# Performance work log

Hardware: AMD Instinct MI355X
Metric: run time of the kernel (lower is better)

Reference implementation:

```python
import jax, jax.numpy as jnp
import numpy as np

N, E, HD, ED = 8000, 40000, 64, 16


def setup_inputs() -> dict:
    key = jax.random.key(0)
    ks = jax.random.split(key, 10)
    def nrm(k, shp, s):
        return jax.random.normal(k, shp, dtype=jnp.float32) * s
    return {
        "x": jax.random.normal(ks[0], (N, HD), dtype=jnp.float32),
        "edge_attr": jax.random.uniform(ks[1], (E, ED), dtype=jnp.float32),
        "W1": nrm(ks[2], (ED, HD), 0.2),
        "b1": jnp.zeros((HD,), jnp.float32),
        "W2": nrm(ks[3], (HD, HD * HD), 0.05),
        "b2": jnp.zeros((HD * HD,), jnp.float32),
        "W_root": nrm(ks[4], (HD, HD), 0.1),
        "b_conv": jnp.zeros((HD,), jnp.float32),
        "w_ih": nrm(ks[5], (3 * HD, HD), 0.1),
        "w_hh": nrm(ks[6], (3 * HD, HD), 0.1),
        "b_ih": jnp.zeros((3 * HD,), jnp.float32),
        "b_hh": jnp.zeros((3 * HD,), jnp.float32),
        "edge_index": jax.random.randint(ks[7], (2, E), 0, N),
    }


def reference(x, edge_attr, W1, b1, W2, b2, W_root, b_conv, w_ih, w_hh, b_ih, b_hh, edge_index):
    src, dst = edge_index[0], edge_index[1]
    n_nodes, hd = x.shape
    n_edges = edge_attr.shape[0]
    # in-degree counts for scatter-mean (guard against isolated nodes)
    counts = jnp.maximum(
        jax.ops.segment_sum(jnp.ones((n_edges,), x.dtype), dst, num_segments=n_nodes), 1.0
    )
    # edge MLP -> per-edge [hd, hd] weight; edge_attr is loop-invariant so compute once
    Wedge = (jax.nn.relu(edge_attr @ W1 + b1) @ W2 + b2).reshape(n_edges, hd, hd)

    def gru_cell(m, h):
        gi = m @ w_ih.T + b_ih  # [N, 3h], gate order r,z,n (torch layout)
        gh = h @ w_hh.T + b_hh
        i_r, i_z, i_n = jnp.split(gi, 3, axis=-1)
        h_r, h_z, h_n = jnp.split(gh, 3, axis=-1)
        r = jax.nn.sigmoid(i_r + h_r)
        z = jax.nn.sigmoid(i_z + h_z)
        n = jnp.tanh(i_n + r * h_n)
        return (1.0 - z) * n + z * h

    out = x
    hidden = x  # h = out.unsqueeze(0)
    for _ in range(3):
        # NNConv: gather source feats, per-edge matmul, scatter-mean to target
        msg = jnp.einsum('ei,eio->eo', out[src], Wedge)  # [E, hd]
        agg = jax.ops.segment_sum(msg, dst, num_segments=n_nodes) / counts[:, None]
        m = jax.nn.relu(agg + out @ W_root.T + b_conv)
        hidden = gru_cell(m, hidden)
        out = hidden  # GRU output == new hidden for seq_len 1
    return out
```

## Files before the change

### kernel.cpp

```cpp
#include <hip/hip_runtime.h>

#define HD 64
#define ED 16

typedef __bf16 bf16x8 __attribute__((ext_vector_type(8)));
typedef float  f32x4  __attribute__((ext_vector_type(4)));
typedef unsigned int u32;
typedef unsigned long long u64;
typedef unsigned short u16;

static inline __device__ float bf2f(u16 u){
    union { u32 i; float f; } v; v.i = ((u32)u) << 16; return v.f;
}
static inline __device__ u16 f2bf(float f){
    union { u32 i; float f; } v; v.f = f;
    u32 r = v.i + 0x7FFF + ((v.i >> 16) & 1);
    return (u16)(r >> 16);
}
static inline __device__ u32 pk2(float a, float b){
    return (u32)f2bf(a) | ((u32)f2bf(b) << 16);
}

__global__ void k_zero2(int* a, int* b, int n){
    int i = blockIdx.x*blockDim.x + threadIdx.x;
    if(i < n){ a[i] = 0; b[i] = 0; }
}
__global__ void k_deg(const int* __restrict__ src, const int* __restrict__ dst, int E,
                      int* __restrict__ degs, int* __restrict__ degd){
    int e = blockIdx.x*blockDim.x + threadIdx.x;
    if(e < E){ atomicAdd(&degs[src[e]], 1); atomicAdd(&degd[dst[e]], 1); }
}

__global__ void k_scan(const int* __restrict__ degs, const int* __restrict__ degd, int N,
                       int* __restrict__ rowptr, int* __restrict__ cursor, float* __restrict__ countsf){
    __shared__ int part[1024];
    int tid = threadIdx.x;
    int PER = (N + 1023) >> 10;
    int base = tid * PER;
    int local[16];
    int s = 0;
    for(int j = 0; j < PER; j++){
        int idx = base + j;
        int v = (idx < N) ? degs[idx] : 0;
        local[j] = s; s += v;
    }
    part[tid] = s;
    __syncthreads();
    for(int off = 1; off < 1024; off <<= 1){
        int v = (tid >= off) ? part[tid - off] : 0;
        __syncthreads();
        part[tid] += v;
        __syncthreads();
    }
    int prev = (tid == 0) ? 0 : part[tid - 1];
    for(int j = 0; j < PER; j++){
        int idx = base + j;
        if(idx < N){
            int r = prev + local[j];
            rowptr[idx] = r; cursor[idx] = r;
            int dd = degd[idx];
            countsf[idx] = (dd > 0) ? (float)dd : 1.0f;
        }
    }
    if(tid == 1023) rowptr[N] = prev + s;
}

__global__ void k_fill(const int* __restrict__ src, int E, int* __restrict__ cursor, int* __restrict__ elist){
    int e = blockIdx.x*blockDim.x + threadIdx.x;
    if(e < E){ int p = atomicAdd(&cursor[src[e]], 1); elist[p] = e; }
}

__global__ void k_h1E(const float* __restrict__ ea, const float* __restrict__ W1,
                      const float* __restrict__ b1, const int* __restrict__ elist,
                      const int* __restrict__ dstarr, int E,
                      u16* __restrict__ h1E, int* __restrict__ dstE){
    __shared__ float s_ea[4][ED];
    __shared__ int s_e[4];
    int t = threadIdx.x;
    int o = t & 63, el = t >> 6;
    int p = blockIdx.x*4 + el;
    if(t < 4){
        int pp = blockIdx.x*4 + t;
        s_e[t] = (pp < E) ? elist[pp] : 0;
    }
    __syncthreads();
    if(t < 4*ED){
        int pe = t/ED;
        s_ea[pe][t%ED] = ea[(size_t)s_e[pe]*ED + t%ED];
    }
    __syncthreads();
    if(p < E){
        float acc = b1[o];
        #pragma unroll
        for(int k = 0; k < ED; k++) acc += s_ea[el][k] * W1[k*HD + o];
        h1E[(size_t)p*HD + o] = f2bf(acc > 0.f ? acc : 0.f);
        if(o == 0) dstE[p] = dstarr[s_e[el]];
    }
}

#define SEG_PT   (65*HD*HD)
#define SEG_WIH  (3*HD*HD)
#define SEG_WHH  (3*HD*HD)
#define SEG_WR   (HD*HD)
__global__ void k_prep(const float* __restrict__ W2, const float* __restrict__ b2,
                       const float* __restrict__ w_ih, const float* __restrict__ w_hh,
                       const float* __restrict__ Wroot, const float* __restrict__ x,
                       u16* __restrict__ PT, u16* __restrict__ WihB, u16* __restrict__ WhhB,
                       u16* __restrict__ WrB, u16* __restrict__ Abf, int nx){
    int idx = blockIdx.x*blockDim.x + threadIdx.x;
    if(idx < SEG_PT){
        int c = idx / HD, i = idx % HD;
        int kc = c >> 6, o = c & 63;
        float v = (kc < HD) ? W2[(size_t)kc*(HD*HD) + i*HD + o] : b2[i*HD + o];
        PT[idx] = f2bf(v);
        return;
    }
    idx -= SEG_PT;
    if(idx < SEG_WIH){ WihB[idx] = f2bf(w_ih[idx]); return; }
    idx -= SEG_WIH;
    if(idx < SEG_WHH){ WhhB[idx] = f2bf(w_hh[idx]); return; }
    idx -= SEG_WHH;
    if(idx < SEG_WR){ WrB[idx] = f2bf(Wroot[idx]); return; }
    idx -= SEG_WR;
    if(idx < nx) Abf[idx] = f2bf(x[idx]);
}

static __device__ __forceinline__ void mfma_row(const u16* __restrict__ Pb,
        int r, int g, bf16x8 a0, bf16x8 a1, f32x4* acc){
    #pragma unroll
    for(int cb = 0; cb < 4; cb++){
        bf16x8 b0 = *(const bf16x8*)&Pb[(cb*16 + r)*HD + g*8];
        bf16x8 b1 = *(const bf16x8*)&Pb[(cb*16 + r)*HD + 32 + g*8];
        acc[cb] = __builtin_amdgcn_mfma_f32_16x16x32_bf16(a0, b0, acc[cb], 0,0,0);
        acc[cb] = __builtin_amdgcn_mfma_f32_16x16x32_bf16(a1, b1, acc[cb], 0,0,0);
    }
}

__global__ __launch_bounds__(256) void k_gemmA4(
        const u16* __restrict__ Abf, const u16* __restrict__ PT,
        u16* __restrict__ Mt, float* __restrict__ Mb, float* __restrict__ agg, int N){
    __shared__ u16 sP[4*HD*HD];
    int t = threadIdx.x;
    int Q = blockIdx.x;
    if(Q == 16){
        int stride = gridDim.y * 256;
        f32x4 z = (f32x4){0.f,0.f,0.f,0.f};
        for(int i = blockIdx.y*256 + t; i < N*HD/4; i += stride)
            *(f32x4*)&agg[i*4] = z;
        return;
    }
    int w = t >> 6, lane = t & 63;
    int r = lane & 15, g = lane >> 4;
    int n0 = (blockIdx.y * 4 + w) * 16;
    size_t NQ = (size_t)N * 256;

    bf16x8 a0 = *(const bf16x8*)&Abf[(size_t)(n0 + r)*HD + g*8];
    bf16x8 a1 = *(const bf16x8*)&Abf[(size_t)(n0 + r)*HD + 32 + g*8];

    {
        const uint4* src = (const uint4*)(PT + (size_t)(Q*4)*HD*HD);
        uint4 tmp0 = src[0*256 + t], tmp1 = src[1*256 + t],
              tmp2 = src[2*256 + t], tmp3 = src[3*256 + t],
              tmp4 = src[4*256 + t], tmp5 = src[5*256 + t],
              tmp6 = src[6*256 + t], tmp7 = src[7*256 + t];
        #define STG(rd, val) { int idx = (rd)*256 + t; int row = idx >> 3, sl = idx & 7; \
            *(uint4*)((char*)sP + row*128 + ((sl ^ (row&7))<<4)) = (val); }
        STG(0, tmp0) STG(1, tmp1) STG(2, tmp2) STG(3, tmp3)
        STG(4, tmp4) STG(5, tmp5) STG(6, tmp6) STG(7, tmp7)
        #undef STG
    }
    __syncthreads();

    f32x4 acc0[4], acc1[4], acc2[4], acc3[4];
    #pragma unroll
    for(int cb = 0; cb < 4; cb++){
        acc0[cb] = (f32x4){0.f,0.f,0.f,0.f};
        acc1[cb] = (f32x4){0.f,0.f,0.f,0.f};
        acc2[cb] = (f32x4){0.f,0.f,0.f,0.f};
        acc3[cb] = (f32x4){0.f,0.f,0.f,0.f};
    }
    #define LDB(j, cb, ks) (*(const bf16x8*)((const char*)sP + \
        ((j)*64 + (cb)*16 + r)*128 + ((((ks)*4 + g) ^ (((cb)*16 + r)&7))<<4)))
    #pragma unroll
    for(int cb = 0; cb < 4; cb++){
        acc0[cb] = __builtin_amdgcn_mfma_f32_16x16x32_bf16(a0, LDB(0,cb,0), acc0[cb], 0,0,0);
        acc0[cb] = __builtin_amdgcn_mfma_f32_16x16x32_bf16(a1, LDB(0,cb,1), acc0[cb], 0,0,0);
        acc1[cb] = __builtin_amdgcn_mfma_f32_16x16x32_bf16(a0, LDB(1,cb,0), acc1[cb], 0,0,0);
        acc1[cb] = __builtin_amdgcn_mfma_f32_16x16x32_bf16(a1, LDB(1,cb,1), acc1[cb], 0,0,0);
        acc2[cb] = __builtin_amdgcn_mfma_f32_16x16x32_bf16(a0, LDB(2,cb,0), acc2[cb], 0,0,0);
        acc2[cb] = __builtin_amdgcn_mfma_f32_16x16x32_bf16(a1, LDB(2,cb,1), acc2[cb], 0,0,0);
        acc3[cb] = __builtin_amdgcn_mfma_f32_16x16x32_bf16(a0, LDB(3,cb,0), acc3[cb], 0,0,0);
        acc3[cb] = __builtin_amdgcn_mfma_f32_16x16x32_bf16(a1, LDB(3,cb,1), acc3[cb], 0,0,0);
    }
    #undef LDB
    #pragma unroll
    for(int cb = 0; cb < 4; cb++){
        int o = cb*16 + r;
        #pragma unroll
        for(int reg = 0; reg < 4; reg++){
            int node = n0 + 4*g + reg;
            u64 v = (u64)pk2(acc0[cb][reg], acc1[cb][reg])
                  | ((u64)pk2(acc2[cb][reg], acc3[cb][reg]) << 32);
            __builtin_nontemporal_store(v,
                (u64*)&Mt[(size_t)Q*NQ + (size_t)node*256 + (size_t)o*4]);
        }
    }
    if(Q == 0){
        f32x4 accB[4];
        #pragma unroll
        for(int cb = 0; cb < 4; cb++) accB[cb] = (f32x4){0.f,0.f,0.f,0.f};
        mfma_row(PT + (size_t)64*HD*HD, r, g, a0, a1, accB);
        #pragma unroll
        for(int cb = 0; cb < 4; cb++)
            #pragma unroll
            for(int reg = 0; reg < 4; reg++)
                Mb[(size_t)(n0 + 4*g + reg)*HD + cb*16 + r] = accB[cb][reg];
    }
}

__global__ __launch_bounds__(256) void k_msgB(
        const u16* __restrict__ Mt, const float* __restrict__ Mb,
        const u16* __restrict__ h1E, const int* __restrict__ rowptr,
        const int* __restrict__ dstE, int E, float* __restrict__ agg, int N){
    int t = threadIdx.x;
    int w = t >> 6, lane = t & 63;
    int r = lane & 15, g = lane >> 4;
    int s = blockIdx.x * 4 + w;
    int beg = rowptr[s], end = rowptr[s+1];
    if(beg == end) return;
    size_t NQ = (size_t)N * 256;

    const u16* Mn = Mt + (size_t)s*256;
    bf16x8 sB[4][2];
    float bval[4];
    #pragma unroll
    for(int cb = 0; cb < 4; cb++){
        int o = cb*16 + r;
        #pragma unroll
        for(int ks = 0; ks < 2; ks++){
            int Qa = ks*8 + 2*g;
            u64 lo = *(const u64*)&Mn[(size_t)Qa*NQ + o*4];
            u64 hi = *(const u64*)&Mn[(size_t)(Qa+1)*NQ + o*4];
            union { u64 q[2]; bf16x8 v; } u;
            u.q[0] = lo; u.q[1] = hi;
            sB[cb][ks] = u.v;
        }
        bval[cb] = Mb[(size_t)s*HD + o];
    }
    for(int p0 = beg; p0 < end; p0 += 16){
        int p = p0 + r;
        int pc = p < E ? p : E-1;
        bf16x8 h0 = *(const bf16x8*)&h1E[(size_t)pc*HD + g*8];
        bf16x8 h1 = *(const bf16x8*)&h1E[(size_t)pc*HD + 32 + g*8];
        f32x4 acc2[4];
        #pragma unroll
        for(int cb = 0; cb < 4; cb++){
            acc2[cb] = (f32x4){0.f,0.f,0.f,0.f};
            acc2[cb] = __builtin_amdgcn_mfma_f32_16x16x32_bf16(h0, sB[cb][0], acc2[cb], 0,0,0);
            acc2[cb] = __builtin_amdgcn_mfma_f32_16x16x32_bf16(h1, sB[cb][1], acc2[cb], 0,0,0);
        }
        int dq[4];
        #pragma unroll
        for(int reg = 0; reg < 4; reg++){
            int q = p0 + 4*g + reg;
            dq[reg] = (q < end) ? dstE[q] : -1;
        }
        #pragma unroll
        for(int cb = 0; cb < 4; cb++)
            #pragma unroll
            for(int reg = 0; reg < 4; reg++)
                if(dq[reg] >= 0)
                    atomicAdd(&agg[(size_t)dq[reg]*HD + cb*16 + r],
                              acc2[cb][reg] + bval[cb]);
    }
}

#define GSTR 201
__global__ __launch_bounds__(256) void k_mgru2(
        const float* __restrict__ agg, const float* __restrict__ countsf,
        const float* __restrict__ state, const u16* __restrict__ Abf,
        const u16* __restrict__ WrB,  const u16* __restrict__ WihB,
        const u16* __restrict__ WhhB, const float* __restrict__ bconv,
        const float* __restrict__ b_ih, const float* __restrict__ b_hh,
        float* __restrict__ hnew, u16* __restrict__ AbfN){
    __shared__ u16   s_mbf[16*72];
    __shared__ float s_gi[16*GSTR];
    __shared__ float s_gh[16*GSTR];
    int t = threadIdx.x;
    int w = t >> 6, lane = t & 63;
    int r = lane & 15, g = lane >> 4;
    int n0 = blockIdx.x * 16;

    bf16x8 afr0 = *(const bf16x8*)&Abf[(size_t)(n0 + r)*HD + g*8];
    bf16x8 afr1 = *(const bf16x8*)&Abf[(size_t)(n0 + r)*HD + 32 + g*8];

    {
        float bc = bconv[w*16 + r];
        f32x4 accR = (f32x4){bc, bc, bc, bc};
        bf16x8 b0 = *(const bf16x8*)&WrB[(size_t)(w*16 + r)*HD + g*8];
        bf16x8 b1 = *(const bf16x8*)&WrB[(size_t)(w*16 + r)*HD + 32 + g*8];
        accR = __builtin_amdgcn_mfma_f32_16x16x32_bf16(afr0, b0, accR, 0,0,0);
        accR = __builtin_amdgcn_mfma_f32_16x16x32_bf16(afr1, b1, accR, 0,0,0);
        #pragma unroll
        for(int reg = 0; reg < 4; reg++){
            int row = 4*g + reg;
            float cnt = countsf[n0 + row];
            float m = agg[(size_t)(n0 + row)*HD + w*16 + r] / cnt + accR[reg];
            s_mbf[row*72 + w*16 + r] = f2bf(m > 0.f ? m : 0.f);
        }
    }
    __syncthreads();

    bf16x8 am0 = *(const bf16x8*)&s_mbf[r*72 + g*8];
    bf16x8 am1 = *(const bf16x8*)&s_mbf[r*72 + 32 + g*8];

    #pragma unroll
    for(int j = 0; j < 3; j++){
        int cb = w + 4*j;
        int col = cb*16 + r;
        float bi = b_ih[col];
        f32x4 acc = (f32x4){bi, bi, bi, bi};
        bf16x8 b0 = *(const bf16x8*)&WihB[(size_t)col*HD + g*8];
        bf16x8 b1 = *(const bf16x8*)&WihB[(size_t)col*HD + 32 + g*8];
        acc = __builtin_amdgcn_mfma_f32_16x16x32_bf16(am0, b0, acc, 0,0,0);
        acc = __builtin_amdgcn_mfma_f32_16x16x32_bf16(am1, b1, acc, 0,0,0);
        #pragma unroll
        for(int reg = 0; reg < 4; reg++)
            s_gi[(4*g + reg)*GSTR + col] = acc[reg];
    }
    #pragma unroll
    for(int j = 0; j < 3; j++){
        int cb = w + 4*j;
        int col = cb*16 + r;
        float bh = b_hh[col];
        f32x4 acc = (f32x4){bh, bh, bh, bh};
        bf16x8 b0 = *(const bf16x8*)&WhhB[(size_t)col*HD + g*8];
        bf16x8 b1 = *(const bf16x8*)&WhhB[(size_t)col*HD + 32 + g*8];
        acc = __builtin_amdgcn_mfma_f32_16x16x32_bf16(afr0, b0, acc, 0,0,0);
        acc = __builtin_amdgcn_mfma_f32_16x16x32_bf16(afr1, b1, acc, 0,0,0);
        #pragma unroll
        for(int reg = 0; reg < 4; reg++)
            s_gh[(4*g + reg)*GSTR + col] = acc[reg];
    }
    __syncthreads();

    #pragma unroll
    for(int q = 0; q < 4; q++){
        int idx = t + q*256;
        int nl = idx >> 6, o = idx & 63;
        const float* gi = s_gi + nl*GSTR;
        const float* gh = s_gh + nl*GSTR;
        float rr  = 1.f/(1.f + __expf(-(gi[o]      + gh[o])));
        float zz  = 1.f/(1.f + __expf(-(gi[64+o]   + gh[64+o])));
        float nnv = tanhf(gi[128+o] + rr*gh[128+o]);
        float xo = state[(size_t)(n0+nl)*HD + o];
        float hh = (1.f - zz)*nnv + zz*xo;
        hnew[(size_t)(n0+nl)*HD + o] = hh;
        AbfN[(size_t)(n0+nl)*HD + o] = f2bf(hh);
    }
}

extern "C" void kernel_launch(void* const* d_in, const int* in_sizes, int n_in,
                              void* d_out, int out_size, void* d_ws, size_t ws_size,
                              hipStream_t stream){
    const float* x     = (const float*)d_in[0];
    const float* ea    = (const float*)d_in[1];
    const float* W1    = (const float*)d_in[2];
    const float* b1    = (const float*)d_in[3];
    const float* W2    = (const float*)d_in[4];
    const float* b2    = (const float*)d_in[5];
    const float* Wroot = (const float*)d_in[6];
    const float* bconv = (const float*)d_in[7];
    const float* w_ih  = (const float*)d_in[8];
    const float* w_hh  = (const float*)d_in[9];
    const float* b_ih  = (const float*)d_in[10];
    const float* b_hh  = (const float*)d_in[11];
    const int*   eidx  = (const int*)d_in[12];
    int N = in_sizes[0] / HD;
    int E = in_sizes[1] / ED;
    const int* srcarr = eidx;
    const int* dstarr = eidx + E;

    char* w = (char*)d_ws;
    size_t off = 0;
    auto alloc = [&](size_t bytes)->char*{
        char* p = w + off; off = (off + bytes + 255) & ~(size_t)255; return p;
    };
    int*   deg_src = (int*)alloc((size_t)N*4);
    int*   deg_dst = (int*)alloc((size_t)N*4);
    int*   rowptr  = (int*)alloc((size_t)(N+1)*4);
    int*   cursor  = (int*)alloc((size_t)N*4);
    int*   elist   = (int*)alloc((size_t)E*4);
    int*   dstE    = (int*)alloc((size_t)E*4);
    float* countsf = (float*)alloc((size_t)N*4);
    u16*   h1E     = (u16*)alloc((size_t)E*HD*2);
    u16*   PT      = (u16*)alloc((size_t)65*HD*HD*2);
    u16*   Abf     = (u16*)alloc((size_t)N*HD*2);
    u16*   WihB    = (u16*)alloc((size_t)3*HD*HD*2);
    u16*   WhhB    = (u16*)alloc((size_t)3*HD*HD*2);
    u16*   WrB     = (u16*)alloc((size_t)HD*HD*2);
    float* agg     = (float*)alloc((size_t)N*HD*4);
    float* stA     = (float*)alloc((size_t)N*HD*4);
    float* stB     = (float*)alloc((size_t)N*HD*4);
    float* Mb      = (float*)alloc((size_t)N*HD*4);
    u16*   Mt      = (u16*)alloc((size_t)N*4096*2);

    hipLaunchKernelGGL(k_zero2, dim3((N+255)/256), dim3(256), 0, stream, deg_src, deg_dst, N);
    hipLaunchKernelGGL(k_deg,   dim3((E+255)/256), dim3(256), 0, stream, srcarr, dstarr, E, deg_src, deg_dst);
    hipLaunchKernelGGL(k_scan,  dim3(1), dim3(1024), 0, stream, deg_src, deg_dst, N, rowptr, cursor, countsf);
    hipLaunchKernelGGL(k_fill,  dim3((E+255)/256), dim3(256), 0, stream, srcarr, E, cursor, elist);
    hipLaunchKernelGGL(k_h1E,   dim3((E+3)/4), dim3(256), 0, stream, ea, W1, b1, elist, dstarr, E, h1E, dstE);
    int prep_total = SEG_PT + SEG_WIH + SEG_WHH + SEG_WR + N*HD;
    hipLaunchKernelGGL(k_prep,  dim3((prep_total+255)/256), dim3(256), 0, stream,
                       W2, b2, w_ih, w_hh, Wroot, x, PT, WihB, WhhB, WrB, Abf, N*HD);

    const float* state = x;
    for(int it = 0; it < 3; ++it){
        hipLaunchKernelGGL(k_gemmA4, dim3(17, N/64), dim3(256), 0, stream, Abf, PT, Mt, Mb, agg, N);
        hipLaunchKernelGGL(k_msgB,  dim3(N/4), dim3(256), 0, stream,
                           Mt, Mb, h1E, rowptr, dstE, E, agg, N);
        float* outp = (it == 2) ? (float*)d_out : ((it == 0) ? stA : stB);
        hipLaunchKernelGGL(k_mgru2, dim3(N/16), dim3(256), 0, stream,
                           agg, countsf, state, Abf, WrB, WihB, WhhB,
                           bconv, b_ih, b_hh, outp, Abf);
        state = outp;
    }
}
```

Measured before the change: 185.5 us.

## Fuse per-node weight GEMM with message kernel via shared-memory staging

Replaces the two-kernel path that wrote a large per-node bf16 matrix Mt (N*4096 elements) to global memory and read it back, with one kernel. It computes each node's 64x64 transformed weights into 160 KB of LDS per 16-node block and consumes them directly for the edge messages. The bias GEMM and agg zeroing become separate small kernels. The aim is to remove the global round trip of Mt. In exchange each block reloads all of PT from global, runs 16 serialized sync phases, and the large LDS footprint limits occupancy to one block per CU.

```diff
diff --git a/kernel.cpp b/kernel.cpp
--- a/kernel.cpp
+++ b/kernel.cpp
@@ -2,6 +2,7 @@
 
 #define HD 64
 #define ED 16
+#define FLDS (16*8192 + 32768)
 
 typedef __bf16 bf16x8 __attribute__((ext_vector_type(8)));
 typedef float  f32x4  __attribute__((ext_vector_type(4)));
@@ -17,13 +18,14 @@
     u32 r = v.i + 0x7FFF + ((v.i >> 16) & 1);
     return (u16)(r >> 16);
 }
-static inline __device__ u32 pk2(float a, float b){
-    return (u32)f2bf(a) | ((u32)f2bf(b) << 16);
-}
 
 __global__ void k_zero2(int* a, int* b, int n){
     int i = blockIdx.x*blockDim.x + threadIdx.x;
     if(i < n){ a[i] = 0; b[i] = 0; }
+}
+__global__ void k_zerof(float* a, int n){
+    int i = blockIdx.x*blockDim.x + threadIdx.x;
+    if(i < n) a[i] = 0.f;
 }
 __global__ void k_deg(const int* __restrict__ src, const int* __restrict__ dst, int E,
                       int* __restrict__ degs, int* __restrict__ degd){
@@ -136,115 +138,82 @@
     }
 }
 
-__global__ __launch_bounds__(256) void k_gemmA4(
-        const u16* __restrict__ Abf, const u16* __restrict__ PT,
-        u16* __restrict__ Mt, float* __restrict__ Mb, float* __restrict__ agg, int N){
-    __shared__ u16 sP[4*HD*HD];
-    int t = threadIdx.x;
-    int Q = blockIdx.x;
-    if(Q == 16){
-        int stride = gridDim.y * 256;
-        f32x4 z = (f32x4){0.f,0.f,0.f,0.f};
-        for(int i = blockIdx.y*256 + t; i < N*HD/4; i += stride)
-            *(f32x4*)&agg[i*4] = z;
-        return;
-    }
-    int w = t >> 6, lane = t & 63;
-    int r = lane & 15, g = lane >> 4;
-    int n0 = (blockIdx.y * 4 + w) * 16;
-    size_t NQ = (size_t)N * 256;
-
-    bf16x8 a0 = *(const bf16x8*)&Abf[(size_t)(n0 + r)*HD + g*8];
-    bf16x8 a1 = *(const bf16x8*)&Abf[(size_t)(n0 + r)*HD + 32 + g*8];
-
-    {
-        const uint4* src = (const uint4*)(PT + (size_t)(Q*4)*HD*HD);
-        uint4 tmp0 = src[0*256 + t], tmp1 = src[1*256 + t],
-              tmp2 = src[2*256 + t], tmp3 = src[3*256 + t],
-              tmp4 = src[4*256 + t], tmp5 = src[5*256 + t],
-              tmp6 = src[6*256 + t], tmp7 = src[7*256 + t];
-        #define STG(rd, val) { int idx = (rd)*256 + t; int row = idx >> 3, sl = idx & 7; \
-            *(uint4*)((char*)sP + row*128 + ((sl ^ (row&7))<<4)) = (val); }
-        STG(0, tmp0) STG(1, tmp1) STG(2, tmp2) STG(3, tmp3)
-        STG(4, tmp4) STG(5, tmp5) STG(6, tmp6) STG(7, tmp7)
-        #undef STG
-    }
-    __syncthreads();
-
-    f32x4 acc0[4], acc1[4], acc2[4], acc3[4];
-    #pragma unroll
-    for(int cb = 0; cb < 4; cb++){
-        acc0[cb] = (f32x4){0.f,0.f,0.f,0.f};
-        acc1[cb] = (f32x4){0.f,0.f,0.f,0.f};
-        acc2[cb] = (f32x4){0.f,0.f,0.f,0.f};
-        acc3[cb] = (f32x4){0.f,0.f,0.f,0.f};
-    }
-    #define LDB(j, cb, ks) (*(const bf16x8*)((const char*)sP + \
-        ((j)*64 + (cb)*16 + r)*128 + ((((ks)*4 + g) ^ (((cb)*16 + r)&7))<<4)))
-    #pragma unroll
-    for(int cb = 0; cb < 4; cb++){
-        acc0[cb] = __builtin_amdgcn_mfma_f32_16x16x32_bf16(a0, LDB(0,cb,0), acc0[cb], 0,0,0);
-        acc0[cb] = __builtin_amdgcn_mfma_f32_16x16x32_bf16(a1, LDB(0,cb,1), acc0[cb], 0,0,0);
-        acc1[cb] = __builtin_amdgcn_mfma_f32_16x16x32_bf16(a0, LDB(1,cb,0), acc1[cb], 0,0,0);
-        acc1[cb] = __builtin_amdgcn_mfma_f32_16x16x32_bf16(a1, LDB(1,cb,1), acc1[cb], 0,0,0);
-        acc2[cb] = __builtin_amdgcn_mfma_f32_16x16x32_bf16(a0, LDB(2,cb,0), acc2[cb], 0,0,0);
-        acc2[cb] = __builtin_amdgcn_mfma_f32_16x16x32_bf16(a1, LDB(2,cb,1), acc2[cb], 0,0,0);
-        acc3[cb] = __builtin_amdgcn_mfma_f32_16x16x32_bf16(a0, LDB(3,cb,0), acc3[cb], 0,0,0);
-        acc3[cb] = __builtin_amdgcn_mfma_f32_16x16x32_bf16(a1, LDB(3,cb,1), acc3[cb], 0,0,0);
-    }
-    #undef LDB
-    #pragma unroll
-    for(int cb = 0; cb < 4; cb++){
-        int o = cb*16 + r;
-        #pragma unroll
-        for(int reg = 0; reg < 4; reg++){
-            int node = n0 + 4*g + reg;
-            u64 v = (u64)pk2(acc0[cb][reg], acc1[cb][reg])
-                  | ((u64)pk2(acc2[cb][reg], acc3[cb][reg]) << 32);
-            __builtin_nontemporal_store(v,
-                (u64*)&Mt[(size_t)Q*NQ + (size_t)node*256 + (size_t)o*4]);
-        }
-    }
-    if(Q == 0){
-        f32x4 accB[4];
-        #pragma unroll
-        for(int cb = 0; cb < 4; cb++) accB[cb] = (f32x4){0.f,0.f,0.f,0.f};
-        mfma_row(PT + (size_t)64*HD*HD, r, g, a0, a1, accB);
-        #pragma unroll
-        for(int cb = 0; cb < 4; cb++)
-            #pragma unroll
-            for(int reg = 0; reg < 4; reg++)
-                Mb[(size_t)(n0 + 4*g + reg)*HD + cb*16 + r] = accB[cb][reg];
-    }
-}
-
-__global__ __launch_bounds__(256) void k_msgB(
-        const u16* __restrict__ Mt, const float* __restrict__ Mb,
-        const u16* __restrict__ h1E, const int* __restrict__ rowptr,
-        const int* __restrict__ dstE, int E, float* __restrict__ agg, int N){
+__global__ __launch_bounds__(256) void k_bias(
+        const u16* __restrict__ Abf, const u16* __restrict__ PT, float* __restrict__ Mb){
     int t = threadIdx.x;
     int w = t >> 6, lane = t & 63;
     int r = lane & 15, g = lane >> 4;
-    int s = blockIdx.x * 4 + w;
+    int n0 = (blockIdx.x * 4 + w) * 16;
+    bf16x8 a0 = *(const bf16x8*)&Abf[(size_t)(n0 + r)*HD + g*8];
+    bf16x8 a1 = *(const bf16x8*)&Abf[(size_t)(n0 + r)*HD + 32 + g*8];
+    f32x4 accB[4];
+    #pragma unroll
+    for(int cb = 0; cb < 4; cb++) accB[cb] = (f32x4){0.f,0.f,0.f,0.f};
+    mfma_row(PT + (size_t)64*HD*HD, r, g, a0, a1, accB);
+    #pragma unroll
+    for(int cb = 0; cb < 4; cb++)
+        #pragma unroll
+        for(int reg = 0; reg < 4; reg++)
+            Mb[(size_t)(n0 + 4*g + reg)*HD + cb*16 + r] = accB[cb][reg];
+}
+
+__global__ __launch_bounds__(1024, 4) void k_fusedM(
+        const u16* __restrict__ Abf, const u16* __restrict__ PT,
+        const u16* __restrict__ h1E, const int* __restrict__ rowptr,
+        const int* __restrict__ dstE, const float* __restrict__ Mb,
+        int E, float* __restrict__ agg){
+    extern __shared__ char smem[];
+    char* S = smem + 16*8192;
+    int t = threadIdx.x;
+    int w = t >> 6, lane = t & 63;
+    int r = lane & 15, g = lane >> 4;
+    int nb0 = blockIdx.x * 16;
+
+    bf16x8 a0 = *(const bf16x8*)&Abf[(size_t)(nb0 + r)*HD + g*8];
+    bf16x8 a1 = *(const bf16x8*)&Abf[(size_t)(nb0 + r)*HD + 32 + g*8];
+
+    int kcl = w >> 2, otile = w & 3;
+    int o1 = otile*16 + r;
+
+    for(int c = 0; c < 16; c++){
+        const uint4* src = (const uint4*)(PT + (size_t)(4*c)*HD*HD);
+        uint4 v0 = src[t], v1 = src[t + 1024];
+        __syncthreads();
+        {
+            int idx = t;      int row = idx >> 3, sl = idx & 7;
+            *(uint4*)(S + row*128 + ((sl ^ (row&7))<<4)) = v0;
+        }
+        {
+            int idx = t+1024; int row = idx >> 3, sl = idx & 7;
+            *(uint4*)(S + row*128 + ((sl ^ (row&7))<<4)) = v1;
+        }
+        __syncthreads();
+        int row0 = kcl*64 + o1;
+        f32x4 acc = (f32x4){0.f,0.f,0.f,0.f};
+        bf16x8 b0 = *(const bf16x8*)(S + row0*128 + (((0*4 + g) ^ (row0&7))<<4));
+        bf16x8 b1 = *(const bf16x8*)(S + row0*128 + (((1*4 + g) ^ (row0&7))<<4));
+        acc = __builtin_amdgcn_mfma_f32_16x16x32_bf16(a0, b0, acc, 0,0,0);
+        acc = __builtin_amdgcn_mfma_f32_16x16x32_bf16(a1, b1, acc, 0,0,0);
+        int kc = 4*c + kcl;
+        int sw = ((((kc>>3) ^ (o1&7))) << 4) + (kc & 7)*2;
+        #pragma unroll
+        for(int reg = 0; reg < 4; reg++)
+            *(u16*)(smem + (4*g + reg)*8192 + o1*128 + sw) = f2bf(acc[reg]);
+    }
+    __syncthreads();
+
+    int s = nb0 + w;
     int beg = rowptr[s], end = rowptr[s+1];
     if(beg == end) return;
-    size_t NQ = (size_t)N * 256;
-
-    const u16* Mn = Mt + (size_t)s*256;
+    const char* Mn = smem + w*8192;
     bf16x8 sB[4][2];
     float bval[4];
     #pragma unroll
     for(int cb = 0; cb < 4; cb++){
         int o = cb*16 + r;
         #pragma unroll
-        for(int ks = 0; ks < 2; ks++){
-            int Qa = ks*8 + 2*g;
-            u64 lo = *(const u64*)&Mn[(size_t)Qa*NQ + o*4];
-            u64 hi = *(const u64*)&Mn[(size_t)(Qa+1)*NQ + o*4];
-            union { u64 q[2]; bf16x8 v; } u;
-            u.q[0] = lo; u.q[1] = hi;
-            sB[cb][ks] = u.v;
-        }
+        for(int ks = 0; ks < 2; ks++)
+            sB[cb][ks] = *(const bf16x8*)(Mn + o*128 + (((ks*4 + g) ^ (o&7))<<4));
         bval[cb] = Mb[(size_t)s*HD + o];
     }
     for(int p0 = beg; p0 < end; p0 += 16){
@@ -400,10 +369,12 @@
     u16*   WhhB    = (u16*)alloc((size_t)3*HD*HD*2);
     u16*   WrB     = (u16*)alloc((size_t)HD*HD*2);
     float* agg     = (float*)alloc((size_t)N*HD*4);
+    float* Mb      = (float*)alloc((size_t)N*HD*4);
     float* stA     = (float*)alloc((size_t)N*HD*4);
     float* stB     = (float*)alloc((size_t)N*HD*4);
-    float* Mb      = (float*)alloc((size_t)N*HD*4);
-    u16*   Mt      = (u16*)alloc((size_t)N*4096*2);
+
+    hipFuncSetAttribute((const void*)k_fusedM,
+                        hipFuncAttributeMaxDynamicSharedMemorySize, FLDS);
 
     hipLaunchKernelGGL(k_zero2, dim3((N+255)/256), dim3(256), 0, stream, deg_src, deg_dst, N);
     hipLaunchKernelGGL(k_deg,   dim3((E+255)/256), dim3(256), 0, stream, srcarr, dstarr, E, deg_src, deg_dst);
@@ -416,9 +387,10 @@
 
     const float* state = x;
     for(int it = 0; it < 3; ++it){
-        hipLaunchKernelGGL(k_gemmA4, dim3(17, N/64), dim3(256), 0, stream, Abf, PT, Mt, Mb, agg, N);
-        hipLaunchKernelGGL(k_msgB,  dim3(N/4), dim3(256), 0, stream,
-                           Mt, Mb, h1E, rowptr, dstE, E, agg, N);
+        hipLaunchKernelGGL(k_zerof, dim3((N*HD+255)/256), dim3(256), 0, stream, agg, N*HD);
+        hipLaunchKernelGGL(k_bias,  dim3(N/64), dim3(256), 0, stream, Abf, PT, Mb);
+        hipLaunchKernelGGL(k_fusedM, dim3(N/16), dim3(1024), FLDS, stream,
+                           Abf, PT, h1E, rowptr, dstE, Mb, E, agg);
         float* outp = (it == 2) ? (float*)d_out : ((it == 0) ? stA : stB);
         hipLaunchKernelGGL(k_mgru2, dim3(N/16), dim3(256), 0, stream,
                            agg, countsf, state, Abf, WrB, WihB, WhhB,
```

Measured after the change: 194.3 us. 1.05x slower.
